# Optimization experiments

Hardware: AMD Instinct MI355X
Metric: run time of the kernel (lower is better)

## Reference

```python
import jax, jax.numpy as jnp
import numpy as np

KH, KW, PAD = 3, 3, 1
K = KH * KW


def _offset_conv(x, w, b):
    # standard 3x3 conv, stride 1, padding 1, NCHW
    out = jax.lax.conv_general_dilated(
        x, w, window_strides=(1, 1), padding=((PAD, PAD), (PAD, PAD)),
        dimension_numbers=("NCHW", "OIHW", "NCHW"))
    return out + b[None, :, None, None]


def _deform_conv(x, offsets, weight, groups):
    # torchvision.ops.deform_conv2d semantics: offset channels are
    # (dy, dx) pairs per kernel tap; zero padding outside the image;
    # bilinear interpolation with per-corner validity masks.
    B, C, H, W = x.shape
    off = offsets.reshape(B, K, 2, H, W)
    dy, dx = off[:, :, 0], off[:, :, 1]                      # [B,K,H,W]

    ky, kx = jnp.meshgrid(jnp.arange(KH), jnp.arange(KW), indexing="ij")
    ky = ky.reshape(K); kx = kx.reshape(K)
    base_y = (jnp.arange(H)[None, :, None] + (ky - PAD)[:, None, None])  # [K,H,1]
    base_x = (jnp.arange(W)[None, None, :] + (kx - PAD)[:, None, None])  # [K,1,W]
    py = base_y[None].astype(x.dtype) + dy                   # [B,K,H,W]
    px = base_x[None].astype(x.dtype) + dx

    # torchvision returns 0 when the sample point is fully outside
    valid = (py > -1) & (py < H) & (px > -1) & (px < W)
    y0 = jnp.floor(py); x0 = jnp.floor(px)
    ly = py - y0; lx = px - x0                               # fractional parts
    y0i = y0.astype(jnp.int32); x0i = x0.astype(jnp.int32)

    def gather(yi, xi):
        ok = (yi >= 0) & (yi < H) & (xi >= 0) & (xi < W) & valid
        yic = jnp.clip(yi, 0, H - 1)
        xic = jnp.clip(xi, 0, W - 1)
        def per_b(img, yb, xb, okb):
            # img [C,H,W]; yb,xb,okb [K,H,W] -> [C,K,H,W]
            return img[:, yb, xb] * okb[None].astype(img.dtype)
        return jax.vmap(per_b)(x, yic, xic, ok)

    v00 = gather(y0i, x0i)
    v01 = gather(y0i, x0i + 1)
    v10 = gather(y0i + 1, x0i)
    v11 = gather(y0i + 1, x0i + 1)
    w00 = ((1 - ly) * (1 - lx))[:, None]
    w01 = ((1 - ly) * lx)[:, None]
    w10 = (ly * (1 - lx))[:, None]
    w11 = (ly * lx)[:, None]
    sampled = v00 * w00 + v01 * w01 + v10 * w10 + v11 * w11  # [B,C,K,H,W]

    Cg = C // groups
    sampled = sampled.reshape(B, groups, Cg, K, H, W)
    wg = weight.reshape(groups, Cg, Cg, K)                   # [G, Cout_g, Cin_g, K]
    out = jnp.einsum("bgckhw,gock->bgohw", sampled, wg)
    return out.reshape(B, C, H, W)


def setup_inputs() -> dict:
    key = jax.random.key(0)
    k1, k2, k3, k4 = jax.random.split(key, 4)
    B, C, H, W, groups = 4, 256, 96, 96, 4
    x = jax.random.normal(k1, (B, C, H, W), dtype=jnp.float32)
    # small offset-conv weights keep learned offsets in a realistic range
    offset_w = jax.random.normal(k2, (2 * K, C, KH, KW), dtype=jnp.float32) * 0.02
    offset_b = jax.random.normal(k3, (2 * K,), dtype=jnp.float32) * 0.1
    fan_in = (C // groups) * KH * KW
    weight = jax.random.normal(k4, (C, C // groups, KH, KW), dtype=jnp.float32) / np.sqrt(fan_in)
    return {"x": x, "offset_w": offset_w, "offset_b": offset_b,
            "weight": weight, "groups": groups}


def reference(x, offset_w, offset_b, weight, groups):
    offsets = _offset_conv(x, offset_w, offset_b)
    return _deform_conv(x, offsets, weight, groups)
```

## Files before the change

kernel.cpp:

```cpp
#include <hip/hip_runtime.h>
#include <hip/hip_bf16.h>
#include <math.h>

#define B_   4
#define C_   256
#define H_   96
#define W_   96
#define HW_  (H_ * W_)
#define G_   4
#define CG_  64
#define K_   9
#define PW_  98
#define PROW_ (PW_ * C_)

typedef __bf16  bf16x8 __attribute__((ext_vector_type(8)));
typedef float   f32x4  __attribute__((ext_vector_type(4)));

__global__ __launch_bounds__(256) void prep_kernel(
    const float* __restrict__ ow, const float* __restrict__ wt,
    __hip_bfloat16* __restrict__ aOW, __hip_bfloat16* __restrict__ aW)
{
    int idx = blockIdx.x * 256 + threadIdx.x;
    if (idx < 73728) {
        int j    = idx & 7;
        int r    = idx >> 3;
        int lane = r & 63;  r >>= 6;
        int mt   = r & 1;   r >>= 1;
        int ks   = r & 7;   r >>= 3;
        int tap  = r;
        int m = mt * 16 + (lane & 15);
        int c = ks * 32 + (lane >> 4) * 8 + j;
        float v = (m < 18) ? ow[(m * 256 + c) * 9 + tap] : 0.f;
        aOW[idx] = __float2bfloat16(v);
    }
    if (idx < 147456) {
        int j    = idx & 7;
        int r    = idx >> 3;
        int lane = r & 63;  r >>= 6;
        int ct   = r & 1;   r >>= 1;
        int half = r & 1;   r >>= 1;
        int ks   = r & 1;   r >>= 1;
        int tap  = r % 9;
        int g    = r / 9;
        int c  = ks * 32 + (lane >> 4) * 8 + j;
        int co = half * 32 + ct * 16 + (lane & 15);
        float v = wt[(((g * CG_ + co) * CG_ + c) * 9) + tap];
        aW[idx] = __float2bfloat16(v);
    }
}

__global__ __launch_bounds__(256) void transpose_kernel(
    const float* __restrict__ x, __hip_bfloat16* __restrict__ xtp)
{
    int blk = blockIdx.x;
    int b = blk / H_, h = blk - b * H_;
    int t = threadIdx.x;
    __shared__ __align__(16) __hip_bfloat16 tile[96 * 264];
    const float* xb = x + (size_t)b * C_ * HW_ + h * W_;
    for (int r = 0; r < 96; ++r) {
        int e = r * 256 + t;
        int c = e / 96, w = e - c * 96;
        tile[w * 264 + c] = __float2bfloat16(xb[c * HW_ + w]);
    }
    __syncthreads();
    __hip_bfloat16* ob = xtp + ((size_t)(b * PW_ + h + 1) * PW_ + 1) * C_;
#pragma unroll
    for (int i = 0; i < 12; ++i) {
        int sIdx = i * 256 + t;
        int px = sIdx >> 5, seg = sIdx & 31;
        *(bf16x8*)(ob + px * 256 + seg * 8) =
            *(const bf16x8*)(&tile[px * 264 + seg * 8]);
    }
    bf16x8 z = {};
    if (t < 64) {
        int side = t >> 5, i = t & 31;
        *(bf16x8*)(xtp + ((size_t)(b * PW_ + h + 1) * PW_ + side * 97) * C_ + i * 8) = z;
    }
    if (h == 0 || h == 95) {
        int row = (h == 0) ? 0 : 97;
        __hip_bfloat16* rb = xtp + (size_t)(b * PW_ + row) * PROW_;
#pragma unroll
        for (int i = 0; i < 13; ++i) {
            int idx = i * 256 + t;
            if (idx < 3136) *(bf16x8*)(rb + idx * 8) = z;
        }
    }
}

__global__ __launch_bounds__(384) void offset_conv_kernel(
    const __hip_bfloat16* __restrict__ xtp, const __hip_bfloat16* __restrict__ aOW,
    const float* __restrict__ bias, __hip_bfloat16* __restrict__ off2)
{
    int blk = blockIdx.x;
    int xcd = blk & 7;
    int s   = blk >> 3;
    int bh  = xcd * 48 + s;
    int b   = bh / H_, h = bh % H_;
    int t = threadIdx.x, lane = t & 63;
    int nt = __builtin_amdgcn_readfirstlane(t >> 6);
    int w0 = nt * 16;
    int ml = lane & 15, kq = lane >> 4;

    f32x4 acc0 = {}, acc1 = {};
    const __hip_bfloat16* xb = xtp + (size_t)b * (PW_ * PROW_);
#pragma unroll
    for (int ky = 0; ky < 3; ++ky) {
#pragma unroll
        for (int kx = 0; kx < 3; ++kx) {
            int tap = ky * 3 + kx;
            const __hip_bfloat16* brow =
                xb + ((h + ky) * PW_ + (w0 + ml + kx)) * C_ + kq * 8;
            const __hip_bfloat16* arow = aOW + tap * 8192 + lane * 8;
#pragma unroll
            for (int ks = 0; ks < 8; ++ks) {
                bf16x8 bf = *(const bf16x8*)(brow + ks * 32);
                bf16x8 a0 = *(const bf16x8*)(arow + ks * 1024);
                bf16x8 a1 = *(const bf16x8*)(arow + ks * 1024 + 512);
                acc0 = __builtin_amdgcn_mfma_f32_16x16x32_bf16(a0, bf, acc0, 0, 0, 0);
                acc1 = __builtin_amdgcn_mfma_f32_16x16x32_bf16(a1, bf, acc1, 0, 0, 0);
            }
        }
    }
    int w = w0 + ml;
#pragma unroll
    for (int r = 0; r < 4; ++r) {
        int j0 = kq * 4 + r;
        off2[((size_t)(b * 9 + (j0 >> 1)) * HW_ + h * W_ + w) * 2 + (j0 & 1)] =
            __float2bfloat16(acc0[r] + bias[j0]);
        int j1 = 16 + kq * 4 + r;
        if (j1 < 18)
            off2[((size_t)(b * 9 + (j1 >> 1)) * HW_ + h * W_ + w) * 2 + (j1 & 1)] =
                __float2bfloat16(acc1[r] + bias[j1]);
    }
}

__global__ __launch_bounds__(384, 4) void deform_kernel(
    const __hip_bfloat16* __restrict__ xtp, const __hip_bfloat16* __restrict__ off2,
    const __hip_bfloat16* __restrict__ aW, float* __restrict__ out)
{
    int blk = blockIdx.x;
    int xcd = blk & 7;
    int s   = blk >> 3;
    int bg  = xcd * 2 + (s / H_);
    int h   = s % H_;
    int g   = bg & 3;
    int b   = bg >> 2;
    int t    = threadIdx.x;
    int lane = t & 63;
    int wave = __builtin_amdgcn_readfirstlane(t >> 6);
    int half   = wave & 1;
    int wthird = wave >> 1;

    __shared__ __align__(16) __hip_bfloat16 sS[2][96 * 72];

    const __hip_bfloat16* xb = xtp + ((size_t)b * (PW_ * PW_) + 99) * C_ + g * CG_;
    const __hip_bfloat162* offp =
        (const __hip_bfloat162*)off2 + (size_t)(b * 9) * HW_ + h * W_;
    const __hip_bfloat16* aWg = aW + (g * 9) * 4096;

    int tw8 = t >> 3;
    int j8  = (t & 7) * 8;

    f32x4 acc[2][2] = {};

    auto sample = [&](int k, int p) {
        int ky = k / 3, kx = k - ky * 3;
#pragma unroll
        for (int it = 0; it < 2; ++it) {
            int w  = it * 48 + tw8;
            __hip_bfloat162 pr = offp[k * HW_ + w];
            float dy = __bfloat162float(pr.x);
            float dx = __bfloat162float(pr.y);
            float py = (float)(h + ky - 1) + dy;
            float px = (float)(w + kx - 1) + dx;
            bool valid = (py > -1.f) && (py < (float)H_) &&
                         (px > -1.f) && (px < (float)W_);
            float y0f = floorf(py), x0f = floorf(px);
            float ly = py - y0f, lx = px - x0f;
            int y0 = (int)y0f, x0 = (int)x0f;
            int y1 = y0 + 1,  x1 = x0 + 1;
            bool y0ok = valid && (y0 >= 0) && (y0 < H_);
            bool y1ok = valid && (y1 >= 0) && (y1 < H_);
            bool x0ok = (x0 >= 0) && (x0 < W_);
            bool x1ok = (x1 >= 0) && (x1 < W_);
            int y0c = min(max(y0, 0), H_ - 1);
            int y1c = min(max(y1, 0), H_ - 1);
            int x0c = min(max(x0, 0), W_ - 1);
            int x1c = min(max(x1, 0), W_ - 1);
            float bw00 = (y0ok && x0ok) ? (1.f - ly) * (1.f - lx) : 0.f;
            float bw01 = (y0ok && x1ok) ? (1.f - ly) * lx : 0.f;
            float bw10 = (y1ok && x0ok) ? ly * (1.f - lx) : 0.f;
            float bw11 = (y1ok && x1ok) ? ly * lx : 0.f;
            bf16x8 c00 = *(const bf16x8*)(xb + (y0c * PW_ + x0c) * C_ + j8);
            bf16x8 c01 = *(const bf16x8*)(xb + (y0c * PW_ + x1c) * C_ + j8);
            bf16x8 c10 = *(const bf16x8*)(xb + (y1c * PW_ + x0c) * C_ + j8);
            bf16x8 c11 = *(const bf16x8*)(xb + (y1c * PW_ + x1c) * C_ + j8);
            bf16x8 r;
#pragma unroll
            for (int e = 0; e < 8; ++e) {
                float v = bw00 * (float)c00[e] + bw01 * (float)c01[e]
                        + bw10 * (float)c10[e] + bw11 * (float)c11[e];
                r[e] = (__bf16)v;
            }
            *(bf16x8*)(&sS[p][w * 72 + j8]) = r;
        }
    };

    auto mmtap = [&](int k, int p) {
        bf16x8 afrag[2][2];
        const __hip_bfloat16* at = aWg + k * 4096 + half * 1024 + lane * 8;
#pragma unroll
        for (int ks = 0; ks < 2; ++ks)
#pragma unroll
            for (int ct = 0; ct < 2; ++ct)
                afrag[ks][ct] = *(const bf16x8*)(at + ks * 2048 + ct * 512);
#pragma unroll
        for (int ks = 0; ks < 2; ++ks) {
#pragma unroll
            for (int wt = 0; wt < 2; ++wt) {
                int wrow = wthird * 32 + wt * 16 + (lane & 15);
                bf16x8 bfrag = *(const bf16x8*)(
                    &sS[p][wrow * 72 + ks * 32 + (lane >> 4) * 8]);
                acc[0][wt] = __builtin_amdgcn_mfma_f32_16x16x32_bf16(
                                 afrag[ks][0], bfrag, acc[0][wt], 0, 0, 0);
                acc[1][wt] = __builtin_amdgcn_mfma_f32_16x16x32_bf16(
                                 afrag[ks][1], bfrag, acc[1][wt], 0, 0, 0);
            }
        }
    };

    sample(0, 0);
    __syncthreads();
    for (int k = 0; k < K_; ++k) {
        if (k < K_ - 1) sample(k + 1, (k + 1) & 1);
        mmtap(k, k & 1);
        __syncthreads();
    }

    float* ob = out + ((b * C_ + g * CG_ + half * 32) * HW_) + h * W_ + wthird * 32;
    int rbase = (lane >> 4) * 4;
    int ncol  = lane & 15;
#pragma unroll
    for (int ct = 0; ct < 2; ++ct)
#pragma unroll
        for (int wt = 0; wt < 2; ++wt)
#pragma unroll
            for (int r = 0; r < 4; ++r)
                __builtin_nontemporal_store(
                    acc[ct][wt][r],
                    ob + (ct * 16 + rbase + r) * HW_ + wt * 16 + ncol);
}

extern "C" void kernel_launch(void* const* d_in, const int* in_sizes, int n_in,
                              void* d_out, int out_size, void* d_ws, size_t ws_size,
                              hipStream_t stream) {
    const float* x    = (const float*)d_in[0];
    const float* ow   = (const float*)d_in[1];
    const float* obi  = (const float*)d_in[2];
    const float* wt   = (const float*)d_in[3];

    __hip_bfloat16* xtp  = (__hip_bfloat16*)d_ws;
    __hip_bfloat16* off2 = xtp + (size_t)B_ * PW_ * PW_ * C_;
    __hip_bfloat16* aW   = off2 + (size_t)B_ * 9 * HW_ * 2;
    __hip_bfloat16* aOW  = aW + 147456;

    prep_kernel<<<576, 256, 0, stream>>>(ow, wt, aOW, aW);
    transpose_kernel<<<B_ * H_, 256, 0, stream>>>(x, xtp);
    offset_conv_kernel<<<B_ * H_, 384, 0, stream>>>(xtp, aOW, obi, off2);
    deform_kernel<<<B_ * G_ * H_, 384, 0, stream>>>(xtp, off2, aW, (float*)d_out);
}
```

Baseline: 194.3 us.

## Sample bilinear values directly into MFMA B fragments, drop shared-memory staging

The deform kernel no longer stages sampled values in LDS with double buffering and barriers. Each lane now gathers and interpolates exactly the values its MFMA B fragment needs, and each wave computes all 64 output channels for its 32 columns. Blocks shrink to 3 waves, and the weight prep layout is reindexed to match the new 4-way channel split. This removes LDS traffic and syncs, at the cost of more registers, redundant offset/weight math per lane, and less latency hiding since sampling and MFMA are no longer overlapped.

```diff
diff --git a/kernel.cpp b/kernel.cpp
--- a/kernel.cpp
+++ b/kernel.cpp
@@ -37,13 +37,12 @@
         int j    = idx & 7;
         int r    = idx >> 3;
         int lane = r & 63;  r >>= 6;
-        int ct   = r & 1;   r >>= 1;
-        int half = r & 1;   r >>= 1;
+        int cq   = r & 3;   r >>= 2;
         int ks   = r & 1;   r >>= 1;
         int tap  = r % 9;
         int g    = r / 9;
         int c  = ks * 32 + (lane >> 4) * 8 + j;
-        int co = half * 32 + ct * 16 + (lane & 15);
+        int co = cq * 16 + (lane & 15);
         float v = wt[(((g * CG_ + co) * CG_ + c) * 9) + tap];
         aW[idx] = __float2bfloat16(v);
     }
@@ -134,7 +133,7 @@
     }
 }
 
-__global__ __launch_bounds__(384, 4) void deform_kernel(
+__global__ __launch_bounds__(192, 3) void deform_kernel(
     const __hip_bfloat16* __restrict__ xtp, const __hip_bfloat16* __restrict__ off2,
     const __hip_bfloat16* __restrict__ aW, float* __restrict__ out)
 {
@@ -145,29 +144,34 @@
     int h   = s % H_;
     int g   = bg & 3;
     int b   = bg >> 2;
-    int t    = threadIdx.x;
-    int lane = t & 63;
-    int wave = __builtin_amdgcn_readfirstlane(t >> 6);
-    int half   = wave & 1;
-    int wthird = wave >> 1;
-
-    __shared__ __align__(16) __hip_bfloat16 sS[2][96 * 72];
-
-    const __hip_bfloat16* xb = xtp + ((size_t)b * (PW_ * PW_) + 99) * C_ + g * CG_;
+    int lane   = threadIdx.x & 63;
+    int wthird = __builtin_amdgcn_readfirstlane(threadIdx.x >> 6);
+    int n  = lane & 15;
+    int kq = lane >> 4;
+
+    const __hip_bfloat16* xb =
+        xtp + ((size_t)b * (PW_ * PW_) + 99) * C_ + g * CG_ + kq * 8;
     const __hip_bfloat162* offp =
         (const __hip_bfloat162*)off2 + (size_t)(b * 9) * HW_ + h * W_;
-    const __hip_bfloat16* aWg = aW + (g * 9) * 4096;
-
-    int tw8 = t >> 3;
-    int j8  = (t & 7) * 8;
-
-    f32x4 acc[2][2] = {};
-
-    auto sample = [&](int k, int p) {
+    const __hip_bfloat16* aWg = aW + (g * 9) * 4096 + lane * 8;
+
+    f32x4 acc[4][2] = {};
+
+    for (int k = 0; k < K_; ++k) {
         int ky = k / 3, kx = k - ky * 3;
-#pragma unroll
-        for (int it = 0; it < 2; ++it) {
-            int w  = it * 48 + tw8;
+
+        bf16x8 afrag[2][4];
+        const __hip_bfloat16* at = aWg + k * 4096;
+#pragma unroll
+        for (int ks = 0; ks < 2; ++ks)
+#pragma unroll
+            for (int cq = 0; cq < 4; ++cq)
+                afrag[ks][cq] = *(const bf16x8*)(at + ks * 2048 + cq * 512);
+
+        bf16x8 bfrag[2][2];
+#pragma unroll
+        for (int wt = 0; wt < 2; ++wt) {
+            int w = wthird * 32 + wt * 16 + n;
             __hip_bfloat162 pr = offp[k * HW_ + w];
             float dy = __bfloat162float(pr.x);
             float dx = __bfloat162float(pr.y);
@@ -191,64 +195,47 @@
             float bw01 = (y0ok && x1ok) ? (1.f - ly) * lx : 0.f;
             float bw10 = (y1ok && x0ok) ? ly * (1.f - lx) : 0.f;
             float bw11 = (y1ok && x1ok) ? ly * lx : 0.f;
-            bf16x8 c00 = *(const bf16x8*)(xb + (y0c * PW_ + x0c) * C_ + j8);
-            bf16x8 c01 = *(const bf16x8*)(xb + (y0c * PW_ + x1c) * C_ + j8);
-            bf16x8 c10 = *(const bf16x8*)(xb + (y1c * PW_ + x0c) * C_ + j8);
-            bf16x8 c11 = *(const bf16x8*)(xb + (y1c * PW_ + x1c) * C_ + j8);
-            bf16x8 r;
-#pragma unroll
-            for (int e = 0; e < 8; ++e) {
-                float v = bw00 * (float)c00[e] + bw01 * (float)c01[e]
-                        + bw10 * (float)c10[e] + bw11 * (float)c11[e];
-                r[e] = (__bf16)v;
-            }
-            *(bf16x8*)(&sS[p][w * 72 + j8]) = r;
-        }
-    };
-
-    auto mmtap = [&](int k, int p) {
-        bf16x8 afrag[2][2];
-        const __hip_bfloat16* at = aWg + k * 4096 + half * 1024 + lane * 8;
-#pragma unroll
-        for (int ks = 0; ks < 2; ++ks)
-#pragma unroll
-            for (int ct = 0; ct < 2; ++ct)
-                afrag[ks][ct] = *(const bf16x8*)(at + ks * 2048 + ct * 512);
-#pragma unroll
-        for (int ks = 0; ks < 2; ++ks) {
-#pragma unroll
-            for (int wt = 0; wt < 2; ++wt) {
-                int wrow = wthird * 32 + wt * 16 + (lane & 15);
-                bf16x8 bfrag = *(const bf16x8*)(
-                    &sS[p][wrow * 72 + ks * 32 + (lane >> 4) * 8]);
-                acc[0][wt] = __builtin_amdgcn_mfma_f32_16x16x32_bf16(
-                                 afrag[ks][0], bfrag, acc[0][wt], 0, 0, 0);
-                acc[1][wt] = __builtin_amdgcn_mfma_f32_16x16x32_bf16(
-                                 afrag[ks][1], bfrag, acc[1][wt], 0, 0, 0);
+            const __hip_bfloat16* p00 = xb + (y0c * PW_ + x0c) * C_;
+            const __hip_bfloat16* p01 = xb + (y0c * PW_ + x1c) * C_;
+            const __hip_bfloat16* p10 = xb + (y1c * PW_ + x0c) * C_;
+            const __hip_bfloat16* p11 = xb + (y1c * PW_ + x1c) * C_;
+#pragma unroll
+            for (int ks = 0; ks < 2; ++ks) {
+                bf16x8 c00 = *(const bf16x8*)(p00 + ks * 32);
+                bf16x8 c01 = *(const bf16x8*)(p01 + ks * 32);
+                bf16x8 c10 = *(const bf16x8*)(p10 + ks * 32);
+                bf16x8 c11 = *(const bf16x8*)(p11 + ks * 32);
+                bf16x8 r;
+#pragma unroll
+                for (int e = 0; e < 8; ++e) {
+                    float v = bw00 * (float)c00[e] + bw01 * (float)c01[e]
+                            + bw10 * (float)c10[e] + bw11 * (float)c11[e];
+                    r[e] = (__bf16)v;
+                }
+                bfrag[wt][ks] = r;
             }
         }
-    };
-
-    sample(0, 0);
-    __syncthreads();
-    for (int k = 0; k < K_; ++k) {
-        if (k < K_ - 1) sample(k + 1, (k + 1) & 1);
-        mmtap(k, k & 1);
-        __syncthreads();
-    }
-
-    float* ob = out + ((b * C_ + g * CG_ + half * 32) * HW_) + h * W_ + wthird * 32;
-    int rbase = (lane >> 4) * 4;
-    int ncol  = lane & 15;
-#pragma unroll
-    for (int ct = 0; ct < 2; ++ct)
+
+#pragma unroll
+        for (int ks = 0; ks < 2; ++ks)
+#pragma unroll
+            for (int wt = 0; wt < 2; ++wt)
+#pragma unroll
+                for (int cq = 0; cq < 4; ++cq)
+                    acc[cq][wt] = __builtin_amdgcn_mfma_f32_16x16x32_bf16(
+                        afrag[ks][cq], bfrag[wt][ks], acc[cq][wt], 0, 0, 0);
+    }
+
+    float* ob = out + ((b * C_ + g * CG_) * HW_) + h * W_ + wthird * 32;
+#pragma unroll
+    for (int cq = 0; cq < 4; ++cq)
 #pragma unroll
         for (int wt = 0; wt < 2; ++wt)
 #pragma unroll
             for (int r = 0; r < 4; ++r)
                 __builtin_nontemporal_store(
-                    acc[ct][wt][r],
-                    ob + (ct * 16 + rbase + r) * HW_ + wt * 16 + ncol);
+                    acc[cq][wt][r],
+                    ob + (cq * 16 + kq * 4 + r) * HW_ + wt * 16 + n);
 }
 
 extern "C" void kernel_launch(void* const* d_in, const int* in_sizes, int n_in,
@@ -267,5 +254,5 @@
     prep_kernel<<<576, 256, 0, stream>>>(ow, wt, aOW, aW);
     transpose_kernel<<<B_ * H_, 256, 0, stream>>>(x, xtp);
     offset_conv_kernel<<<B_ * H_, 384, 0, stream>>>(xtp, aOW, obi, off2);
-    deform_kernel<<<B_ * G_ * H_, 384, 0, stream>>>(xtp, off2, aW, (float*)d_out);
-}
+    deform_kernel<<<B_ * G_ * H_, 192, 0, stream>>>(xtp, off2, aW, (float*)d_out);
+}
```

After: 218.4 us. 1.12x slower.

## Split offset-conv channel reduction across waves; precompute bilinear coefficients in LDS

Applied to the files above, without the earlier changes.

The offset conv kernel now runs 768 threads per block. Two wave groups each reduce half of the input channels, and the partial accumulators are combined through shared memory, so each wave has half as many serial MFMA steps. Separately, the deform kernel computes bilinear weights and corner offsets for all 9 taps × 96 columns once per block into LDS. Before, eight threads per pixel recomputed them redundantly inside the sampling loop. The cost is extra LDS (about 27 KB), an added barrier, and possible occupancy limits on the deform kernel.

```diff
diff --git a/kernel.cpp b/kernel.cpp
--- a/kernel.cpp
+++ b/kernel.cpp
@@ -87,7 +87,7 @@
     }
 }
 
-__global__ __launch_bounds__(384) void offset_conv_kernel(
+__global__ __launch_bounds__(768) void offset_conv_kernel(
     const __hip_bfloat16* __restrict__ xtp, const __hip_bfloat16* __restrict__ aOW,
     const float* __restrict__ bias, __hip_bfloat16* __restrict__ off2)
 {
@@ -97,7 +97,9 @@
     int bh  = xcd * 48 + s;
     int b   = bh / H_, h = bh % H_;
     int t = threadIdx.x, lane = t & 63;
-    int nt = __builtin_amdgcn_readfirstlane(t >> 6);
+    int ww = __builtin_amdgcn_readfirstlane(t >> 6);
+    int nt = ww % 6;
+    int kh = ww / 6;
     int w0 = nt * 16;
     int ml = lane & 15, kq = lane >> 4;
 
@@ -109,10 +111,10 @@
         for (int kx = 0; kx < 3; ++kx) {
             int tap = ky * 3 + kx;
             const __hip_bfloat16* brow =
-                xb + ((h + ky) * PW_ + (w0 + ml + kx)) * C_ + kq * 8;
-            const __hip_bfloat16* arow = aOW + tap * 8192 + lane * 8;
-#pragma unroll
-            for (int ks = 0; ks < 8; ++ks) {
+                xb + ((h + ky) * PW_ + (w0 + ml + kx)) * C_ + kh * 128 + kq * 8;
+            const __hip_bfloat16* arow = aOW + tap * 8192 + kh * 4096 + lane * 8;
+#pragma unroll
+            for (int ks = 0; ks < 4; ++ks) {
                 bf16x8 bf = *(const bf16x8*)(brow + ks * 32);
                 bf16x8 a0 = *(const bf16x8*)(arow + ks * 1024);
                 bf16x8 a1 = *(const bf16x8*)(arow + ks * 1024 + 512);
@@ -121,16 +123,28 @@
             }
         }
     }
-    int w = w0 + ml;
-#pragma unroll
-    for (int r = 0; r < 4; ++r) {
-        int j0 = kq * 4 + r;
-        off2[((size_t)(b * 9 + (j0 >> 1)) * HW_ + h * W_ + w) * 2 + (j0 & 1)] =
-            __float2bfloat16(acc0[r] + bias[j0]);
-        int j1 = 16 + kq * 4 + r;
-        if (j1 < 18)
-            off2[((size_t)(b * 9 + (j1 >> 1)) * HW_ + h * W_ + w) * 2 + (j1 & 1)] =
-                __float2bfloat16(acc1[r] + bias[j1]);
+    __shared__ __align__(16) f32x4 red[6 * 64 * 2];
+    if (kh == 1) {
+        red[(nt * 64 + lane) * 2 + 0] = acc0;
+        red[(nt * 64 + lane) * 2 + 1] = acc1;
+    }
+    __syncthreads();
+    if (kh == 0) {
+        f32x4 r0 = red[(nt * 64 + lane) * 2 + 0];
+        f32x4 r1 = red[(nt * 64 + lane) * 2 + 1];
+        acc0 += r0;
+        acc1 += r1;
+        int w = w0 + ml;
+#pragma unroll
+        for (int r = 0; r < 4; ++r) {
+            int j0 = kq * 4 + r;
+            off2[((size_t)(b * 9 + (j0 >> 1)) * HW_ + h * W_ + w) * 2 + (j0 & 1)] =
+                __float2bfloat16(acc0[r] + bias[j0]);
+            int j1 = 16 + kq * 4 + r;
+            if (j1 < 18)
+                off2[((size_t)(b * 9 + (j1 >> 1)) * HW_ + h * W_ + w) * 2 + (j1 & 1)] =
+                    __float2bfloat16(acc1[r] + bias[j1]);
+        }
     }
 }
 
@@ -152,6 +166,8 @@
     int wthird = wave >> 1;
 
     __shared__ __align__(16) __hip_bfloat16 sS[2][96 * 72];
+    __shared__ __align__(16) f32x4 bwt[864];
+    __shared__ __align__(16) int4  oft[864];
 
     const __hip_bfloat16* xb = xtp + ((size_t)b * (PW_ * PW_) + 99) * C_ + g * CG_;
     const __hip_bfloat162* offp =
@@ -161,46 +177,62 @@
     int tw8 = t >> 3;
     int j8  = (t & 7) * 8;
 
+    for (int e = t; e < 864; e += 384) {
+        int k = e / 96, w = e - (e / 96) * 96;
+        int ky = k / 3, kx = k - ky * 3;
+        __hip_bfloat162 pr = offp[k * HW_ + w];
+        float dy = __bfloat162float(pr.x);
+        float dx = __bfloat162float(pr.y);
+        float py = (float)(h + ky - 1) + dy;
+        float px = (float)(w + kx - 1) + dx;
+        bool valid = (py > -1.f) && (py < (float)H_) &&
+                     (px > -1.f) && (px < (float)W_);
+        float y0f = floorf(py), x0f = floorf(px);
+        float ly = py - y0f, lx = px - x0f;
+        int y0 = (int)y0f, x0 = (int)x0f;
+        int y1 = y0 + 1,  x1 = x0 + 1;
+        bool y0ok = valid && (y0 >= 0) && (y0 < H_);
+        bool y1ok = valid && (y1 >= 0) && (y1 < H_);
+        bool x0ok = (x0 >= 0) && (x0 < W_);
+        bool x1ok = (x1 >= 0) && (x1 < W_);
+        int y0c = min(max(y0, 0), H_ - 1);
+        int y1c = min(max(y1, 0), H_ - 1);
+        int x0c = min(max(x0, 0), W_ - 1);
+        int x1c = min(max(x1, 0), W_ - 1);
+        f32x4 bw;
+        bw[0] = (y0ok && x0ok) ? (1.f - ly) * (1.f - lx) : 0.f;
+        bw[1] = (y0ok && x1ok) ? (1.f - ly) * lx : 0.f;
+        bw[2] = (y1ok && x0ok) ? ly * (1.f - lx) : 0.f;
+        bw[3] = (y1ok && x1ok) ? ly * lx : 0.f;
+        bwt[e] = bw;
+        oft[e] = make_int4((y0c * PW_ + x0c) * C_,
+                           (x1c - x0c) * C_,
+                           (y1c - y0c) * PROW_, 0);
+    }
+
     f32x4 acc[2][2] = {};
 
     auto sample = [&](int k, int p) {
-        int ky = k / 3, kx = k - ky * 3;
 #pragma unroll
         for (int it = 0; it < 2; ++it) {
             int w  = it * 48 + tw8;
-            __hip_bfloat162 pr = offp[k * HW_ + w];
-            float dy = __bfloat162float(pr.x);
-            float dx = __bfloat162float(pr.y);
-            float py = (float)(h + ky - 1) + dy;
-            float px = (float)(w + kx - 1) + dx;
-            bool valid = (py > -1.f) && (py < (float)H_) &&
-                         (px > -1.f) && (px < (float)W_);
-            float y0f = floorf(py), x0f = floorf(px);
-            float ly = py - y0f, lx = px - x0f;
-            int y0 = (int)y0f, x0 = (int)x0f;
-            int y1 = y0 + 1,  x1 = x0 + 1;
-            bool y0ok = valid && (y0 >= 0) && (y0 < H_);
-            bool y1ok = valid && (y1 >= 0) && (y1 < H_);
-            bool x0ok = (x0 >= 0) && (x0 < W_);
-            bool x1ok = (x1 >= 0) && (x1 < W_);
-            int y0c = min(max(y0, 0), H_ - 1);
-            int y1c = min(max(y1, 0), H_ - 1);
-            int x0c = min(max(x0, 0), W_ - 1);
-            int x1c = min(max(x1, 0), W_ - 1);
-            float bw00 = (y0ok && x0ok) ? (1.f - ly) * (1.f - lx) : 0.f;
-            float bw01 = (y0ok && x1ok) ? (1.f - ly) * lx : 0.f;
-            float bw10 = (y1ok && x0ok) ? ly * (1.f - lx) : 0.f;
-            float bw11 = (y1ok && x1ok) ? ly * lx : 0.f;
-            bf16x8 c00 = *(const bf16x8*)(xb + (y0c * PW_ + x0c) * C_ + j8);
-            bf16x8 c01 = *(const bf16x8*)(xb + (y0c * PW_ + x1c) * C_ + j8);
-            bf16x8 c10 = *(const bf16x8*)(xb + (y1c * PW_ + x0c) * C_ + j8);
-            bf16x8 c11 = *(const bf16x8*)(xb + (y1c * PW_ + x1c) * C_ + j8);
+            int e  = k * 96 + w;
+            f32x4 bw = bwt[e];
+            int4  of = oft[e];
+            const __hip_bfloat16* p00 = xb + of.x;
+            const __hip_bfloat16* p01 = xb + of.x + of.y;
+            const __hip_bfloat16* p10 = xb + of.x + of.z;
+            const __hip_bfloat16* p11 = xb + of.x + of.y + of.z;
+            bf16x8 c00 = *(const bf16x8*)(p00 + j8);
+            bf16x8 c01 = *(const bf16x8*)(p01 + j8);
+            bf16x8 c10 = *(const bf16x8*)(p10 + j8);
+            bf16x8 c11 = *(const bf16x8*)(p11 + j8);
             bf16x8 r;
 #pragma unroll
-            for (int e = 0; e < 8; ++e) {
-                float v = bw00 * (float)c00[e] + bw01 * (float)c01[e]
-                        + bw10 * (float)c10[e] + bw11 * (float)c11[e];
-                r[e] = (__bf16)v;
+            for (int e2 = 0; e2 < 8; ++e2) {
+                float v = bw[0] * (float)c00[e2] + bw[1] * (float)c01[e2]
+                        + bw[2] * (float)c10[e2] + bw[3] * (float)c11[e2];
+                r[e2] = (__bf16)v;
             }
             *(bf16x8*)(&sS[p][w * 72 + j8]) = r;
         }
@@ -229,6 +261,7 @@
         }
     };
 
+    __syncthreads();
     sample(0, 0);
     __syncthreads();
     for (int k = 0; k < K_; ++k) {
@@ -266,6 +299,6 @@
 
     prep_kernel<<<576, 256, 0, stream>>>(ow, wt, aOW, aW);
     transpose_kernel<<<B_ * H_, 256, 0, stream>>>(x, xtp);
-    offset_conv_kernel<<<B_ * H_, 384, 0, stream>>>(xtp, aOW, obi, off2);
+    offset_conv_kernel<<<B_ * H_, 768, 0, stream>>>(xtp, aOW, obi, off2);
     deform_kernel<<<B_ * G_ * H_, 384, 0, stream>>>(xtp, off2, aW, (float*)d_out);
 }
```

Measured after the change: 200.0 us. 1.03x slower.

## Split offset conv K across wave pairs with LDS weights; simplify deform bilinear addressing

Applied to the files above, without the earlier changes.

The offset conv kernel doubles its block to 768 threads. The 256-channel reduction is split between two wave halves, and each half accumulates 128 channels. Per-tap weights are double-buffered into LDS, and the two halves' partial sums are combined through shared memory before the write. The deform sampling drops the per-corner clamping and instead relies on the padded transposed input. Invalid samples point to a zero padding position and get zero weights, which cuts address arithmetic and branches in the gather. The cost is extra barriers and LDS in the offset conv, and the deform change depends on the padding covering every reachable corner.

```diff
diff --git a/kernel.cpp b/kernel.cpp
--- a/kernel.cpp
+++ b/kernel.cpp
@@ -87,7 +87,7 @@
     }
 }
 
-__global__ __launch_bounds__(384) void offset_conv_kernel(
+__global__ __launch_bounds__(768) void offset_conv_kernel(
     const __hip_bfloat16* __restrict__ xtp, const __hip_bfloat16* __restrict__ aOW,
     const float* __restrict__ bias, __hip_bfloat16* __restrict__ off2)
 {
@@ -97,40 +97,62 @@
     int bh  = xcd * 48 + s;
     int b   = bh / H_, h = bh % H_;
     int t = threadIdx.x, lane = t & 63;
-    int nt = __builtin_amdgcn_readfirstlane(t >> 6);
+    int ww = __builtin_amdgcn_readfirstlane(t >> 6);
+    int nt = ww % 6;
+    int kh = ww / 6;
     int w0 = nt * 16;
     int ml = lane & 15, kq = lane >> 4;
 
+    __shared__ __align__(16) __hip_bfloat16 aS[2][8192];
+    __shared__ __align__(16) f32x4 red[6 * 64 * 2];
+
+    auto stage = [&](int tap, int p) {
+        const bf16x8* src = (const bf16x8*)(aOW + tap * 8192);
+        bf16x8* dst = (bf16x8*)aS[p];
+        for (int i = t; i < 1024; i += 768) dst[i] = src[i];
+    };
+
     f32x4 acc0 = {}, acc1 = {};
     const __hip_bfloat16* xb = xtp + (size_t)b * (PW_ * PROW_);
-#pragma unroll
-    for (int ky = 0; ky < 3; ++ky) {
-#pragma unroll
-        for (int kx = 0; kx < 3; ++kx) {
-            int tap = ky * 3 + kx;
-            const __hip_bfloat16* brow =
-                xb + ((h + ky) * PW_ + (w0 + ml + kx)) * C_ + kq * 8;
-            const __hip_bfloat16* arow = aOW + tap * 8192 + lane * 8;
-#pragma unroll
-            for (int ks = 0; ks < 8; ++ks) {
-                bf16x8 bf = *(const bf16x8*)(brow + ks * 32);
-                bf16x8 a0 = *(const bf16x8*)(arow + ks * 1024);
-                bf16x8 a1 = *(const bf16x8*)(arow + ks * 1024 + 512);
-                acc0 = __builtin_amdgcn_mfma_f32_16x16x32_bf16(a0, bf, acc0, 0, 0, 0);
-                acc1 = __builtin_amdgcn_mfma_f32_16x16x32_bf16(a1, bf, acc1, 0, 0, 0);
-            }
-        }
-    }
-    int w = w0 + ml;
-#pragma unroll
-    for (int r = 0; r < 4; ++r) {
-        int j0 = kq * 4 + r;
-        off2[((size_t)(b * 9 + (j0 >> 1)) * HW_ + h * W_ + w) * 2 + (j0 & 1)] =
-            __float2bfloat16(acc0[r] + bias[j0]);
-        int j1 = 16 + kq * 4 + r;
-        if (j1 < 18)
-            off2[((size_t)(b * 9 + (j1 >> 1)) * HW_ + h * W_ + w) * 2 + (j1 & 1)] =
-                __float2bfloat16(acc1[r] + bias[j1]);
+
+    stage(0, 0);
+    __syncthreads();
+    for (int tap = 0; tap < 9; ++tap) {
+        if (tap < 8) stage(tap + 1, (tap + 1) & 1);
+        int ky = tap / 3, kx = tap - ky * 3;
+        const __hip_bfloat16* brow =
+            xb + ((h + ky) * PW_ + (w0 + ml + kx)) * C_ + kh * 128 + kq * 8;
+        const __hip_bfloat16* arow = aS[tap & 1] + kh * 4096 + lane * 8;
+#pragma unroll
+        for (int ks = 0; ks < 4; ++ks) {
+            bf16x8 bf = *(const bf16x8*)(brow + ks * 32);
+            bf16x8 a0 = *(const bf16x8*)(arow + ks * 1024);
+            bf16x8 a1 = *(const bf16x8*)(arow + ks * 1024 + 512);
+            acc0 = __builtin_amdgcn_mfma_f32_16x16x32_bf16(a0, bf, acc0, 0, 0, 0);
+            acc1 = __builtin_amdgcn_mfma_f32_16x16x32_bf16(a1, bf, acc1, 0, 0, 0);
+        }
+        __syncthreads();
+    }
+
+    if (kh == 1) {
+        red[(nt * 64 + lane) * 2 + 0] = acc0;
+        red[(nt * 64 + lane) * 2 + 1] = acc1;
+    }
+    __syncthreads();
+    if (kh == 0) {
+        acc0 += red[(nt * 64 + lane) * 2 + 0];
+        acc1 += red[(nt * 64 + lane) * 2 + 1];
+        int w = w0 + ml;
+#pragma unroll
+        for (int r = 0; r < 4; ++r) {
+            int j0 = kq * 4 + r;
+            off2[((size_t)(b * 9 + (j0 >> 1)) * HW_ + h * W_ + w) * 2 + (j0 & 1)] =
+                __float2bfloat16(acc0[r] + bias[j0]);
+            int j1 = 16 + kq * 4 + r;
+            if (j1 < 18)
+                off2[((size_t)(b * 9 + (j1 >> 1)) * HW_ + h * W_ + w) * 2 + (j1 & 1)] =
+                    __float2bfloat16(acc1[r] + bias[j1]);
+        }
     }
 }
 
@@ -153,7 +175,8 @@
 
     __shared__ __align__(16) __hip_bfloat16 sS[2][96 * 72];
 
-    const __hip_bfloat16* xb = xtp + ((size_t)b * (PW_ * PW_) + 99) * C_ + g * CG_;
+    const __hip_bfloat16* xb =
+        xtp + ((size_t)b * (PW_ * PW_) + PW_ + 1) * C_ + g * CG_;
     const __hip_bfloat162* offp =
         (const __hip_bfloat162*)off2 + (size_t)(b * 9) * HW_ + h * W_;
     const __hip_bfloat16* aWg = aW + (g * 9) * 4096;
@@ -169,32 +192,24 @@
         for (int it = 0; it < 2; ++it) {
             int w  = it * 48 + tw8;
             __hip_bfloat162 pr = offp[k * HW_ + w];
-            float dy = __bfloat162float(pr.x);
-            float dx = __bfloat162float(pr.y);
-            float py = (float)(h + ky - 1) + dy;
-            float px = (float)(w + kx - 1) + dx;
+            float py = (float)(h + ky - 1) + __bfloat162float(pr.x);
+            float px = (float)(w + kx - 1) + __bfloat162float(pr.y);
             bool valid = (py > -1.f) && (py < (float)H_) &&
                          (px > -1.f) && (px < (float)W_);
             float y0f = floorf(py), x0f = floorf(px);
             float ly = py - y0f, lx = px - x0f;
             int y0 = (int)y0f, x0 = (int)x0f;
-            int y1 = y0 + 1,  x1 = x0 + 1;
-            bool y0ok = valid && (y0 >= 0) && (y0 < H_);
-            bool y1ok = valid && (y1 >= 0) && (y1 < H_);
-            bool x0ok = (x0 >= 0) && (x0 < W_);
-            bool x1ok = (x1 >= 0) && (x1 < W_);
-            int y0c = min(max(y0, 0), H_ - 1);
-            int y1c = min(max(y1, 0), H_ - 1);
-            int x0c = min(max(x0, 0), W_ - 1);
-            int x1c = min(max(x1, 0), W_ - 1);
-            float bw00 = (y0ok && x0ok) ? (1.f - ly) * (1.f - lx) : 0.f;
-            float bw01 = (y0ok && x1ok) ? (1.f - ly) * lx : 0.f;
-            float bw10 = (y1ok && x0ok) ? ly * (1.f - lx) : 0.f;
-            float bw11 = (y1ok && x1ok) ? ly * lx : 0.f;
-            bf16x8 c00 = *(const bf16x8*)(xb + (y0c * PW_ + x0c) * C_ + j8);
-            bf16x8 c01 = *(const bf16x8*)(xb + (y0c * PW_ + x1c) * C_ + j8);
-            bf16x8 c10 = *(const bf16x8*)(xb + (y1c * PW_ + x0c) * C_ + j8);
-            bf16x8 c11 = *(const bf16x8*)(xb + (y1c * PW_ + x1c) * C_ + j8);
+            int base = valid ? (y0 * PW_ + x0) * C_ : -(PW_ + 1) * C_;
+            float wy1 = valid ? ly : 0.f;
+            float wy0 = valid ? (1.f - ly) : 0.f;
+            float mx0 = 1.f - lx;
+            float bw00 = wy0 * mx0, bw01 = wy0 * lx;
+            float bw10 = wy1 * mx0, bw11 = wy1 * lx;
+            const __hip_bfloat16* p0 = xb + base + j8;
+            bf16x8 c00 = *(const bf16x8*)(p0);
+            bf16x8 c01 = *(const bf16x8*)(p0 + C_);
+            bf16x8 c10 = *(const bf16x8*)(p0 + PROW_);
+            bf16x8 c11 = *(const bf16x8*)(p0 + PROW_ + C_);
             bf16x8 r;
 #pragma unroll
             for (int e = 0; e < 8; ++e) {
@@ -266,6 +281,6 @@
 
     prep_kernel<<<576, 256, 0, stream>>>(ow, wt, aOW, aW);
     transpose_kernel<<<B_ * H_, 256, 0, stream>>>(x, xtp);
-    offset_conv_kernel<<<B_ * H_, 384, 0, stream>>>(xtp, aOW, obi, off2);
+    offset_conv_kernel<<<B_ * H_, 768, 0, stream>>>(xtp, aOW, obi, off2);
     deform_kernel<<<B_ * G_ * H_, 384, 0, stream>>>(xtp, off2, aW, (float*)d_out);
 }
```

Measured after the change: 177.4 us. 8.7% less time.
